# Kernel optimization log

Measured on AMD Instinct MI355X. Metric: run time of the kernel, lower is better.

## Reference

```python
import jax, jax.numpy as jnp
import numpy as np


def _d2(a, b):
    # squared euclidean distances, clamped at 0 (matches _full_cdist before sqrt)
    a2 = jnp.sum(a * a, axis=1)[:, None]
    b2 = jnp.sum(b * b, axis=1)[None, :]
    return jnp.clip(a2 + b2 - 2.0 * (a @ b.T), 0.0, None)


def _node_weights(pts, w1, b1, w2, b2):
    h = jax.nn.relu(pts @ w1 + b1)
    logits = h @ w2 + b2
    w = jax.nn.softplus(logits) + 1e-6
    w = w / jnp.sum(w)
    return w[:, 0]


def setup_inputs() -> dict:
    key = jax.random.key(0)
    ks = jax.random.split(key, 8)
    N, M, D, H, S = 8192, 8192, 2, 32, 3
    return {
        "base_points": jax.random.normal(ks[0], (N, D), jnp.float32),
        "target_points": jax.random.normal(ks[1], (M, D), jnp.float32),
        "log_sigmas": jnp.log(jnp.array([0.05, 0.1, 0.2], jnp.float32)),
        "log_scale": 0.1 * jax.random.normal(ks[2], (D,), jnp.float32),
        "wn_w1": jax.random.normal(ks[3], (D, H), jnp.float32) / np.sqrt(D),
        "wn_b1": jnp.zeros((H,), jnp.float32),
        "wn_w2": jax.random.normal(ks[4], (H, 1), jnp.float32) / np.sqrt(H),
        "wn_b2": jnp.zeros((1,), jnp.float32),
        "g_w1": jax.random.normal(ks[5], (4, H), jnp.float32) / 2.0,
        "g_b1": jnp.zeros((H,), jnp.float32),
        "g_w2": jax.random.normal(ks[6], (H, S), jnp.float32) / np.sqrt(H),
        "g_b2": jnp.zeros((S,), jnp.float32),
        "bias": jnp.zeros((1,), jnp.float32),
    }


def reference(base_points, target_points, log_sigmas, log_scale,
              wn_w1, wn_b1, wn_w2, wn_b2,
              g_w1, g_b1, g_w2, g_b2, bias):
    # learned anisotropic per-axis scale
    scale = jnp.exp(log_scale)
    base = base_points * scale
    target = target_points * scale

    # learned positive, normalized node weights (shared weight_net)
    w_b = _node_weights(base, wn_w1, wn_b1, wn_w2, wn_b2)
    w_t = _node_weights(target, wn_w1, wn_b1, wn_w2, wn_b2)

    # kde_mmd_loss with center=True: subtract weighted mean of each cloud.
    bc = base - jnp.sum(w_b[:, None] * base, axis=0)
    tc = target - jnp.sum(w_t[:, None] * target, axis=0)

    # squared distances computed ONCE, reused across all sigma bands
    d2_aa = _d2(bc, bc)
    d2_bb = _d2(tc, tc)
    d2_ab = _d2(bc, tc)

    sigmas = jnp.exp(log_sigmas)

    def band_loss(sigma):
        inv = 1.0 / (2.0 * sigma * sigma)
        kaa = jnp.exp(-d2_aa * inv)
        kbb = jnp.exp(-d2_bb * inv)
        kab = jnp.exp(-d2_ab * inv)
        # weighted MMD^2: w_a K_aa w_a + w_b K_bb w_b - 2 w_a K_ab w_b
        return (w_b @ (kaa @ w_b) + w_t @ (kbb @ w_t)
                - 2.0 * (w_b @ (kab @ w_t)))

    per_band = jnp.stack([band_loss(sigmas[i]) for i in range(sigmas.shape[0])])

    # gating statistics (torch.tensor([...]) detaches -> stop_gradient)
    dist = jnp.sqrt(_d2(base, target))
    mean_dist = jnp.mean(dist)
    var_dist = jnp.var(dist, ddof=1)  # torch .var() is unbiased
    n_base = base_points.shape[0]
    size_diff = abs(float(n_base - target_points.shape[0])) / (n_base + 1e-6)
    weight_var = jnp.var(w_b, ddof=1) + jnp.var(w_t, ddof=1)
    stats = jax.lax.stop_gradient(
        jnp.stack([mean_dist, var_dist,
                   jnp.asarray(size_diff, base.dtype), weight_var]))

    mix_logits = jax.nn.relu(stats @ g_w1 + g_b1) @ g_w2 + g_b2
    gw = jax.nn.softplus(mix_logits)
    gw = gw / jnp.sum(gw)
    return jnp.sum(gw * per_band) + bias[0]
```

## Files before the change

kernel.cpp:

```cpp
#include <hip/hip_runtime.h>
#include <math.h>

#if __has_builtin(__builtin_amdgcn_exp2f)
#define EXP2F(x) __builtin_amdgcn_exp2f(x)
#else
#define EXP2F(x) exp2f(x)
#endif
#if __has_builtin(__builtin_amdgcn_sqrtf)
#define SQRTF(x) __builtin_amdgcn_sqrtf(x)
#else
#define SQRTF(x) sqrtf(x)
#endif

#define NPTS 8192
#define NJ 512
#define TI 512
#define T16 16
#define NTRI 136
#define NBLK (256 + 2 * NTRI)
#define L2E 1.4426950408889634f

__device__ inline double wred_d(double v) {
#pragma unroll
  for (int o = 32; o > 0; o >>= 1) v += __shfl_down(v, o, 64);
  return v;
}

__device__ inline double bred(double v, double* sm) {
  v = wred_d(v);
  __syncthreads();
  if ((threadIdx.x & 63) == 0) sm[threadIdx.x >> 6] = v;
  __syncthreads();
  return sm[0] + sm[1] + sm[2] + sm[3];
}

__device__ inline void slot_reduce(const double* slot, double* smean) {
  if (threadIdx.x < 64) {
    int l = threadIdx.x;
    const double* sl = slot + l * 4;
#pragma unroll
    for (int c = 0; c < 4; ++c) {
      double v = sl[c];
      double vb = (l < 32) ? v : 0.0;
      double vt = (l < 32) ? 0.0 : v;
      vb = wred_d(vb);
      vt = wred_d(vt);
      if (l == 0) {
        smean[c] = vb;
        smean[4 + c] = vt;
      }
    }
  }
}

__global__ __launch_bounds__(256) void prep_kernel(
    const float* __restrict__ base, const float* __restrict__ target,
    const float* __restrict__ log_sigmas, const float* __restrict__ log_scale,
    const float* __restrict__ w1, const float* __restrict__ b1,
    const float* __restrict__ w2, const float* __restrict__ b2,
    float2* __restrict__ pxy, float* __restrict__ pu,
    double* __restrict__ slot, unsigned* __restrict__ ctr, int n) {
  __shared__ double sm[4];
  int gid = blockIdx.x * 256 + threadIdx.x;
  int isT = gid >= n;
  const float* pts = isT ? target : base;
  int idx = isT ? gid - n : gid;
  float ex = __expf(log_scale[0]);
  float ey = __expf(log_scale[1]);
  float s2 = __expf(log_sigmas[2]);
  float r2 = __fsqrt_rn(L2E / (2.f * s2 * s2));
  float2 p = ((const float2*)pts)[idx];
  float xr = p.x * ex, yr = p.y * ey;
  float logit = b2[0];
#pragma unroll
  for (int k = 0; k < 32; ++k) {
    float h = fmaf(xr, w1[k], fmaf(yr, w1[32 + k], b1[k]));
    h = fmaxf(h, 0.f);
    logit = fmaf(h, w2[k], logit);
  }
  float u = fmaxf(logit, 0.f) + log1pf(__expf(-fabsf(logit))) + 1e-6f;
  float X = xr * r2, Y = yr * r2;
  pxy[gid] = make_float2(X, Y);
  pu[gid] = u;
  double su = bred((double)u, sm);
  double qu = bred((double)u * (double)u, sm);
  double mx = bred((double)u * (double)X, sm);
  double my = bred((double)u * (double)Y, sm);
  if (threadIdx.x == 0) {
    double* s = slot + blockIdx.x * 4;
    s[0] = su;
    s[1] = qu;
    s[2] = mx;
    s[3] = my;
    if (blockIdx.x == 0) *ctr = 0u;
  }
}

template <bool AB, bool FAST>
__device__ inline void tile_loop(const float4* sxy4, const float2* su2,
                                 const float2* sb2, float x0, float y0,
                                 float x1, float y1, float al0, float al1,
                                 float rr0, float rr1, float acc[2][3],
                                 float& sdo, float& sqo) {
  float sd = 0.f, sq = 0.f;
#pragma unroll 2
  for (int jj = 0; jj < NJ / 2; ++jj) {
    float4 xy = sxy4[jj];
    float2 u2 = su2[jj];
    float bj[2];
    if constexpr (AB) {
      float2 b2v = sb2[jj];
      bj[0] = b2v.x;
      bj[1] = b2v.y;
    }
    float xj[2] = {xy.x, xy.z};
    float yj[2] = {xy.y, xy.w};
    float uj[2] = {u2.x, u2.y};
#pragma unroll
    for (int q = 0; q < 2; ++q) {
#pragma unroll
      for (int i = 0; i < 2; ++i) {
        float dx = (i ? x1 : x0) - xj[q];
        float dy = (i ? y1 : y0) - yj[q];
        float s = fmaf(dy, dy, dx * dx);
        float k2 = EXP2F(-s);
        float k0, k1;
        if constexpr (FAST) {
          float t = k2 * k2;
          k1 = t * t;
          float t1 = k1 * k1;
          k0 = t1 * t1;
        } else {
          k1 = EXP2F(-s * rr1);
          k0 = EXP2F(-s * rr0);
        }
        acc[i][0] = fmaf(uj[q], k0, acc[i][0]);
        acc[i][1] = fmaf(uj[q], k1, acc[i][1]);
        acc[i][2] = fmaf(uj[q], k2, acc[i][2]);
        if constexpr (AB) {
          float d2u = fmaxf((s + (i ? al1 : al0)) - bj[q], 0.f);
          sd += SQRTF(d2u);
          sq += d2u;
        }
      }
    }
  }
  sdo = sd;
  sqo = sq;
}

__global__ __launch_bounds__(256) void pair_kernel(
    const float2* __restrict__ pxy, const float* __restrict__ pu,
    const double* __restrict__ slot, double* __restrict__ paa,
    double* __restrict__ pbb, double* __restrict__ pab,
    double* __restrict__ psd, double* __restrict__ psq,
    unsigned* __restrict__ ctr, const float* __restrict__ log_sigmas,
    const float* __restrict__ g_w1, const float* __restrict__ g_b1,
    const float* __restrict__ g_w2, const float* __restrict__ g_b2,
    const float* __restrict__ bias, float* __restrict__ out, int n) {
  __shared__ __align__(16) float2 sxy[NJ];
  __shared__ float su[NJ];
  __shared__ float sb[NJ];
  __shared__ double sm[4];
  __shared__ double smean[8];
  __shared__ int lastf;

  int b = blockIdx.x, m, it, jt, pidx;
  if (b < 256) {
    m = 2;
    pidx = b;
    it = b >> 4;
    jt = b & 15;
  } else {
    int r = b - 256;
    m = (r < NTRI) ? 0 : 1;
    pidx = (m == 0) ? r : r - NTRI;
    int idx = pidx;
    it = 0;
    for (;;) {
      int len = T16 - it;
      if (idx < len) {
        jt = it + idx;
        break;
      }
      idx -= len;
      ++it;
    }
  }
  const float2* pxyI = pxy + ((m == 1) ? n : 0);
  const float* puI = pu + ((m == 1) ? n : 0);
  const float2* pxyJ = pxy + ((m == 0) ? 0 : n);
  const float* puJ = pu + ((m == 0) ? 0 : n);

  int j0 = jt * NJ;
  for (int t = threadIdx.x; t < NJ; t += 256) {
    sxy[t] = pxyJ[j0 + t];
    su[t] = puJ[j0 + t];
  }
  if (m == 2) slot_reduce(slot, smean);
  __syncthreads();

  float cx = 0.f, cy = 0.f;
  if (m == 2) {
    cx = (float)(smean[2] / smean[0] - smean[6] / smean[4]);
    cy = (float)(smean[3] / smean[0] - smean[7] / smean[4]);
    for (int t = threadIdx.x; t < NJ; t += 256) {
      float2 v = sxy[t];
      sb[t] = 2.f * fmaf(cx, v.x, cy * v.y);
    }
    __syncthreads();
  }

  int i0 = it * TI + threadIdx.x;
  float2 P0 = pxyI[i0], P1 = pxyI[i0 + 256];
  float u0 = puI[i0], u1 = puI[i0 + 256];
  float x0 = P0.x - cx, y0 = P0.y - cy;
  float x1 = P1.x - cx, y1 = P1.y - cy;
  float al0 = fmaf(2.f * cx, x0, 2.f * cy * y0) + cx * cx + cy * cy;
  float al1 = fmaf(2.f * cx, x1, 2.f * cy * y1) + cx * cx + cy * cy;

  float s0 = __expf(log_sigmas[0]);
  float s1 = __expf(log_sigmas[1]);
  float s2 = __expf(log_sigmas[2]);
  float rr0 = (s2 * s2) / (s0 * s0);
  float rr1 = (s2 * s2) / (s1 * s1);
  bool fast = (fabsf(rr0 - 16.f) <= 0.016f) && (fabsf(rr1 - 4.f) <= 0.004f);

  float acc[2][3] = {};
  float sd = 0.f, sq = 0.f;
  const float4* sxy4 = reinterpret_cast<const float4*>(sxy);
  const float2* su2 = reinterpret_cast<const float2*>(su);
  const float2* sb2 = reinterpret_cast<const float2*>(sb);
  if (m == 2) {
    if (fast)
      tile_loop<true, true>(sxy4, su2, sb2, x0, y0, x1, y1, al0, al1, rr0, rr1,
                            acc, sd, sq);
    else
      tile_loop<true, false>(sxy4, su2, sb2, x0, y0, x1, y1, al0, al1, rr0,
                             rr1, acc, sd, sq);
  } else {
    if (fast)
      tile_loop<false, true>(sxy4, su2, sb2, x0, y0, x1, y1, al0, al1, rr0,
                             rr1, acc, sd, sq);
    else
      tile_loop<false, false>(sxy4, su2, sb2, x0, y0, x1, y1, al0, al1, rr0,
                              rr1, acc, sd, sq);
  }

  double wgt = (m != 2 && it != jt) ? 2.0 : 1.0;
  double c0 = (double)u0 * (double)acc[0][0] + (double)u1 * (double)acc[1][0];
  double c1 = (double)u0 * (double)acc[0][1] + (double)u1 * (double)acc[1][1];
  double c2 = (double)u0 * (double)acc[0][2] + (double)u1 * (double)acc[1][2];
  double r0 = bred(c0, sm) * wgt;
  double r1 = bred(c1, sm) * wgt;
  double r2d = bred(c2, sm) * wgt;
  double* prow = (m == 0) ? paa : (m == 1) ? pbb : pab;
  int stride = (m == 2) ? 256 : NTRI;
  if (threadIdx.x == 0) {
    prow[0 * stride + pidx] = r0;
    prow[1 * stride + pidx] = r1;
    prow[2 * stride + pidx] = r2d;
  }
  if (m == 2) {
    double rsd = bred((double)sd, sm);
    double rsq = bred((double)sq, sm);
    if (threadIdx.x == 0) {
      psd[pidx] = rsd;
      psq[pidx] = rsq;
    }
  }

  if (threadIdx.x == 0) {
    __threadfence();
    unsigned old = atomicAdd(ctr, 1u);
    lastf = (old == NBLK - 1) ? 1 : 0;
  }
  __syncthreads();
  if (lastf == 0) return;
  __threadfence();

  slot_reduce(slot, smean);
  __syncthreads();
  int t = threadIdx.x;
  double vaa[3], vbb[3], vab[3];
  for (int s = 0; s < 3; ++s) {
    vaa[s] = bred((t < NTRI) ? paa[s * NTRI + t] : 0.0, sm);
    vbb[s] = bred((t < NTRI) ? pbb[s * NTRI + t] : 0.0, sm);
    vab[s] = bred(pab[s * 256 + t], sm);
  }
  double sdt = bred(psd[t], sm);
  double sqt = bred(psq[t], sm);

  if (threadIdx.x == 0) {
    double Sb = smean[0], Qb = smean[1], St = smean[4], Qt = smean[5];
    double pband[3];
    for (int s = 0; s < 3; ++s)
      pband[s] = vaa[s] / (Sb * Sb) + vbb[s] / (St * St) -
                 2.0 * vab[s] / (Sb * St);
    double s2d = (double)s2;
    double r2sq = (double)L2E / (2.0 * s2d * s2d);
    double sd_real = sdt / sqrt(r2sq);
    double sq_real = sqt / r2sq;
    double NN = (double)n;
    double NM = NN * NN;
    double mean_d = sd_real / NM;
    double var_d = (sq_real - sd_real * sd_real / NM) / (NM - 1.0);
    double wv = (Qb / (Sb * Sb) - 1.0 / NN) / (NN - 1.0) +
                (Qt / (St * St) - 1.0 / NN) / (NN - 1.0);
    float st[4] = {(float)mean_d, (float)var_d, 0.f, (float)wv};
    float gl[3] = {g_b2[0], g_b2[1], g_b2[2]};
    for (int k = 0; k < 32; ++k) {
      float h = g_b1[k];
      for (int c = 0; c < 4; ++c) h = fmaf(st[c], g_w1[c * 32 + k], h);
      h = fmaxf(h, 0.f);
      for (int s = 0; s < 3; ++s) gl[s] = fmaf(h, g_w2[k * 3 + s], gl[s]);
    }
    float gw[3];
    float gsum = 0.f;
    for (int s = 0; s < 3; ++s) {
      gw[s] = fmaxf(gl[s], 0.f) + log1pf(__expf(-fabsf(gl[s])));
      gsum += gw[s];
    }
    double r = 0.0;
    for (int s = 0; s < 3; ++s) r += (double)(gw[s] / gsum) * pband[s];
    out[0] = (float)(r + (double)bias[0]);
  }
}

extern "C" void kernel_launch(void* const* d_in, const int* in_sizes, int n_in,
                              void* d_out, int out_size, void* d_ws,
                              size_t ws_size, hipStream_t stream) {
  const float* base = (const float*)d_in[0];
  const float* target = (const float*)d_in[1];
  const float* log_sigmas = (const float*)d_in[2];
  const float* log_scale = (const float*)d_in[3];
  const float* wn_w1 = (const float*)d_in[4];
  const float* wn_b1 = (const float*)d_in[5];
  const float* wn_w2 = (const float*)d_in[6];
  const float* wn_b2 = (const float*)d_in[7];
  const float* g_w1 = (const float*)d_in[8];
  const float* g_b1 = (const float*)d_in[9];
  const float* g_w2 = (const float*)d_in[10];
  const float* g_b2 = (const float*)d_in[11];
  const float* bias = (const float*)d_in[12];
  int n = in_sizes[0] / 2;

  double* dbase = (double*)d_ws;
  double* slot = dbase;
  double* paa = dbase + 256;
  double* pbb = paa + 3 * NTRI;
  double* pab = pbb + 3 * NTRI;
  double* psd = pab + 3 * 256;
  double* psq = psd + 256;
  double* dend = psq + 256;
  float2* pxy = (float2*)dend;
  float* pu = (float*)(pxy + 2 * n);
  unsigned* ctr = (unsigned*)(pu + 2 * n);

  prep_kernel<<<(2 * n) / 256, 256, 0, stream>>>(
      base, target, log_sigmas, log_scale, wn_w1, wn_b1, wn_w2, wn_b2, pxy, pu,
      slot, ctr, n);
  pair_kernel<<<NBLK, 256, 0, stream>>>(pxy, pu, slot, paa, pbb, pab, psd, psq,
                                        ctr, log_sigmas, g_w1, g_b1, g_w2,
                                        g_b2, bias, (float*)d_out, n);
}
```

Measured before the change: 165.9 us.

## Use persistent blocks with atomic job queue and fine-grained 64-column tiles

Replaces the fixed grid of 528 blocks (each handling a 512x512 tile) with 1024 persistent blocks that pull small 512x64 jobs from a global atomic counter. Partial sums are accumulated into a few global doubles with atomicAdd instead of per-block slots reduced by the last block. The aim is better load balance and occupancy across CUs. In exchange it adds per-job synchronisation, reduction and atomic overhead, plus more redundant loading of the i-side points.

```diff
diff --git a/kernel.cpp b/kernel.cpp
--- a/kernel.cpp
+++ b/kernel.cpp
@@ -13,12 +13,16 @@
 #endif
 
 #define NPTS 8192
-#define NJ 512
-#define TI 512
+#define JT 64
+#define ITILE 512
 #define T16 16
 #define NTRI 136
-#define NBLK (256 + 2 * NTRI)
+#define NJOB_AB 2048
+#define NJOB_TRI 1088
+#define NJOBS (NJOB_AB + 2 * NJOB_TRI)
+#define NBLK_PAIR 1024
 #define L2E 1.4426950408889634f
+
 
 __device__ inline double wred_d(double v) {
 #pragma unroll
@@ -59,7 +63,8 @@
     const float* __restrict__ w1, const float* __restrict__ b1,
     const float* __restrict__ w2, const float* __restrict__ b2,
     float2* __restrict__ pxy, float* __restrict__ pu,
-    double* __restrict__ slot, unsigned* __restrict__ ctr, int n) {
+    double* __restrict__ slot, double* __restrict__ acc,
+    unsigned* __restrict__ jctr, unsigned* __restrict__ fctr, int n) {
   __shared__ double sm[4];
   int gid = blockIdx.x * 256 + threadIdx.x;
   int isT = gid >= n;
@@ -92,7 +97,11 @@
     s[1] = qu;
     s[2] = mx;
     s[3] = my;
-    if (blockIdx.x == 0) *ctr = 0u;
+    if (blockIdx.x == 0) {
+      for (int i = 0; i < 11; ++i) acc[i] = 0.0;
+      *jctr = 0u;
+      *fctr = 0u;
+    }
   }
 }
 
@@ -104,7 +113,7 @@
                                  float& sdo, float& sqo) {
   float sd = 0.f, sq = 0.f;
 #pragma unroll 2
-  for (int jj = 0; jj < NJ / 2; ++jj) {
+  for (int jj = 0; jj < JT / 2; ++jj) {
     float4 xy = sxy4[jj];
     float2 u2 = su2[jj];
     float bj[2];
@@ -149,75 +158,28 @@
   sqo = sq;
 }
 
-__global__ __launch_bounds__(256) void pair_kernel(
+__global__ __launch_bounds__(256, 4) void pair_kernel(
     const float2* __restrict__ pxy, const float* __restrict__ pu,
-    const double* __restrict__ slot, double* __restrict__ paa,
-    double* __restrict__ pbb, double* __restrict__ pab,
-    double* __restrict__ psd, double* __restrict__ psq,
-    unsigned* __restrict__ ctr, const float* __restrict__ log_sigmas,
-    const float* __restrict__ g_w1, const float* __restrict__ g_b1,
-    const float* __restrict__ g_w2, const float* __restrict__ g_b2,
-    const float* __restrict__ bias, float* __restrict__ out, int n) {
-  __shared__ __align__(16) float2 sxy[NJ];
-  __shared__ float su[NJ];
-  __shared__ float sb[NJ];
+    const double* __restrict__ slot, double* __restrict__ acc,
+    unsigned* __restrict__ jctr, unsigned* __restrict__ fctr,
+    const float* __restrict__ log_sigmas, const float* __restrict__ g_w1,
+    const float* __restrict__ g_b1, const float* __restrict__ g_w2,
+    const float* __restrict__ g_b2, const float* __restrict__ bias,
+    float* __restrict__ out, int n) {
+  __shared__ __align__(16) float2 sxy[JT];
+  __shared__ __align__(16) float su[JT];
+  __shared__ __align__(16) float sb[JT];
   __shared__ double sm[4];
   __shared__ double smean[8];
+  __shared__ int sjid;
   __shared__ int lastf;
 
-  int b = blockIdx.x, m, it, jt, pidx;
-  if (b < 256) {
-    m = 2;
-    pidx = b;
-    it = b >> 4;
-    jt = b & 15;
-  } else {
-    int r = b - 256;
-    m = (r < NTRI) ? 0 : 1;
-    pidx = (m == 0) ? r : r - NTRI;
-    int idx = pidx;
-    it = 0;
-    for (;;) {
-      int len = T16 - it;
-      if (idx < len) {
-        jt = it + idx;
-        break;
-      }
-      idx -= len;
-      ++it;
-    }
-  }
-  const float2* pxyI = pxy + ((m == 1) ? n : 0);
-  const float* puI = pu + ((m == 1) ? n : 0);
-  const float2* pxyJ = pxy + ((m == 0) ? 0 : n);
-  const float* puJ = pu + ((m == 0) ? 0 : n);
-
-  int j0 = jt * NJ;
-  for (int t = threadIdx.x; t < NJ; t += 256) {
-    sxy[t] = pxyJ[j0 + t];
-    su[t] = puJ[j0 + t];
-  }
-  if (m == 2) slot_reduce(slot, smean);
+  slot_reduce(slot, smean);
   __syncthreads();
-
-  float cx = 0.f, cy = 0.f;
-  if (m == 2) {
-    cx = (float)(smean[2] / smean[0] - smean[6] / smean[4]);
-    cy = (float)(smean[3] / smean[0] - smean[7] / smean[4]);
-    for (int t = threadIdx.x; t < NJ; t += 256) {
-      float2 v = sxy[t];
-      sb[t] = 2.f * fmaf(cx, v.x, cy * v.y);
-    }
-    __syncthreads();
-  }
-
-  int i0 = it * TI + threadIdx.x;
-  float2 P0 = pxyI[i0], P1 = pxyI[i0 + 256];
-  float u0 = puI[i0], u1 = puI[i0 + 256];
-  float x0 = P0.x - cx, y0 = P0.y - cy;
-  float x1 = P1.x - cx, y1 = P1.y - cy;
-  float al0 = fmaf(2.f * cx, x0, 2.f * cy * y0) + cx * cx + cy * cy;
-  float al1 = fmaf(2.f * cx, x1, 2.f * cy * y1) + cx * cx + cy * cy;
+  float cx = (float)(smean[2] / smean[0] - smean[6] / smean[4]);
+  float cy = (float)(smean[3] / smean[0] - smean[7] / smean[4]);
+  float cx2 = 2.f * cx, cy2 = 2.f * cy;
+  float cc = cx * cx + cy * cy;
 
   float s0 = __expf(log_sigmas[0]);
   float s1 = __expf(log_sigmas[1]);
@@ -226,81 +188,122 @@
   float rr1 = (s2 * s2) / (s1 * s1);
   bool fast = (fabsf(rr0 - 16.f) <= 0.016f) && (fabsf(rr1 - 4.f) <= 0.004f);
 
-  float acc[2][3] = {};
-  float sd = 0.f, sq = 0.f;
-  const float4* sxy4 = reinterpret_cast<const float4*>(sxy);
-  const float2* su2 = reinterpret_cast<const float2*>(su);
-  const float2* sb2 = reinterpret_cast<const float2*>(sb);
-  if (m == 2) {
-    if (fast)
-      tile_loop<true, true>(sxy4, su2, sb2, x0, y0, x1, y1, al0, al1, rr0, rr1,
-                            acc, sd, sq);
-    else
-      tile_loop<true, false>(sxy4, su2, sb2, x0, y0, x1, y1, al0, al1, rr0,
-                             rr1, acc, sd, sq);
-  } else {
-    if (fast)
-      tile_loop<false, true>(sxy4, su2, sb2, x0, y0, x1, y1, al0, al1, rr0,
-                             rr1, acc, sd, sq);
-    else
-      tile_loop<false, false>(sxy4, su2, sb2, x0, y0, x1, y1, al0, al1, rr0,
-                              rr1, acc, sd, sq);
-  }
-
-  double wgt = (m != 2 && it != jt) ? 2.0 : 1.0;
-  double c0 = (double)u0 * (double)acc[0][0] + (double)u1 * (double)acc[1][0];
-  double c1 = (double)u0 * (double)acc[0][1] + (double)u1 * (double)acc[1][1];
-  double c2 = (double)u0 * (double)acc[0][2] + (double)u1 * (double)acc[1][2];
-  double r0 = bred(c0, sm) * wgt;
-  double r1 = bred(c1, sm) * wgt;
-  double r2d = bred(c2, sm) * wgt;
-  double* prow = (m == 0) ? paa : (m == 1) ? pbb : pab;
-  int stride = (m == 2) ? 256 : NTRI;
-  if (threadIdx.x == 0) {
-    prow[0 * stride + pidx] = r0;
-    prow[1 * stride + pidx] = r1;
-    prow[2 * stride + pidx] = r2d;
-  }
-  if (m == 2) {
-    double rsd = bred((double)sd, sm);
-    double rsq = bred((double)sq, sm);
+  for (;;) {
+    __syncthreads();
+    if (threadIdx.x == 0) sjid = (int)atomicAdd(jctr, 1u);
+    __syncthreads();
+    int job = sjid;
+    if (job >= NJOBS) break;
+
+    int m, it, jt = 0, j0;
+    if (job < NJOB_AB) {
+      m = 2;
+      it = job >> 7;
+      j0 = (job & 127) * JT;
+    } else {
+      int r = job - NJOB_AB;
+      m = (r < NJOB_TRI) ? 0 : 1;
+      if (m == 1) r -= NJOB_TRI;
+      int tri = r >> 3;
+      int q = r & 7;
+      int idx = tri, len = T16;
+      it = 0;
+      while (idx >= len) {
+        idx -= len;
+        --len;
+        ++it;
+      }
+      jt = it + idx;
+      j0 = jt * ITILE + q * JT;
+    }
+    const float2* pxyI = pxy + ((m == 1) ? n : 0);
+    const float* puI = pu + ((m == 1) ? n : 0);
+    const float2* pxyJ = pxy + ((m == 0) ? 0 : n);
+    const float* puJ = pu + ((m == 0) ? 0 : n);
+
+    if (threadIdx.x < JT) {
+      float2 v = pxyJ[j0 + threadIdx.x];
+      sxy[threadIdx.x] = v;
+      su[threadIdx.x] = puJ[j0 + threadIdx.x];
+      if (m == 2) sb[threadIdx.x] = fmaf(cx2, v.x, cy2 * v.y);
+    }
+    __syncthreads();
+
+    int i0 = it * ITILE + threadIdx.x;
+    float2 P0 = pxyI[i0], P1 = pxyI[i0 + 256];
+    float u0 = puI[i0], u1 = puI[i0 + 256];
+    float x0 = P0.x, y0 = P0.y, x1 = P1.x, y1 = P1.y;
+    float al0 = 0.f, al1 = 0.f;
+    if (m == 2) {
+      x0 -= cx; y0 -= cy; x1 -= cx; y1 -= cy;
+      al0 = fmaf(cx2, x0, cy2 * y0) + cc;
+      al1 = fmaf(cx2, x1, cy2 * y1) + cc;
+    }
+
+    float accf[2][3] = {};
+    float sd = 0.f, sq = 0.f;
+    const float4* sxy4 = reinterpret_cast<const float4*>(sxy);
+    const float2* su2 = reinterpret_cast<const float2*>(su);
+    const float2* sb2 = reinterpret_cast<const float2*>(sb);
+    if (m == 2) {
+      if (fast)
+        tile_loop<true, true>(sxy4, su2, sb2, x0, y0, x1, y1, al0, al1, rr0,
+                              rr1, accf, sd, sq);
+      else
+        tile_loop<true, false>(sxy4, su2, sb2, x0, y0, x1, y1, al0, al1, rr0,
+                               rr1, accf, sd, sq);
+    } else {
+      if (fast)
+        tile_loop<false, true>(sxy4, su2, sb2, x0, y0, x1, y1, al0, al1, rr0,
+                               rr1, accf, sd, sq);
+      else
+        tile_loop<false, false>(sxy4, su2, sb2, x0, y0, x1, y1, al0, al1, rr0,
+                                rr1, accf, sd, sq);
+    }
+
+    double wgt = (m != 2 && jt != it) ? 2.0 : 1.0;
+    double c0 = (double)u0 * accf[0][0] + (double)u1 * accf[1][0];
+    double c1 = (double)u0 * accf[0][1] + (double)u1 * accf[1][1];
+    double c2 = (double)u0 * accf[0][2] + (double)u1 * accf[1][2];
+    double r0 = bred(c0, sm) * wgt;
+    double r1 = bred(c1, sm) * wgt;
+    double r2d = bred(c2, sm) * wgt;
     if (threadIdx.x == 0) {
-      psd[pidx] = rsd;
-      psq[pidx] = rsq;
+      atomicAdd(&acc[3 * m + 0], r0);
+      atomicAdd(&acc[3 * m + 1], r1);
+      atomicAdd(&acc[3 * m + 2], r2d);
+    }
+    if (m == 2) {
+      double rsd = bred((double)sd, sm);
+      double rsq = bred((double)sq, sm);
+      if (threadIdx.x == 0) {
+        atomicAdd(&acc[9], rsd);
+        atomicAdd(&acc[10], rsq);
+      }
     }
   }
 
   if (threadIdx.x == 0) {
     __threadfence();
-    unsigned old = atomicAdd(ctr, 1u);
-    lastf = (old == NBLK - 1) ? 1 : 0;
+    unsigned old = atomicAdd(fctr, 1u);
+    lastf = (old == NBLK_PAIR - 1) ? 1 : 0;
   }
   __syncthreads();
-  if (lastf == 0) return;
+  if (!lastf) return;
   __threadfence();
 
-  slot_reduce(slot, smean);
-  __syncthreads();
-  int t = threadIdx.x;
-  double vaa[3], vbb[3], vab[3];
-  for (int s = 0; s < 3; ++s) {
-    vaa[s] = bred((t < NTRI) ? paa[s * NTRI + t] : 0.0, sm);
-    vbb[s] = bred((t < NTRI) ? pbb[s * NTRI + t] : 0.0, sm);
-    vab[s] = bred(pab[s * 256 + t], sm);
-  }
-  double sdt = bred(psd[t], sm);
-  double sqt = bred(psq[t], sm);
-
   if (threadIdx.x == 0) {
+    double v[11];
+    for (int i = 0; i < 11; ++i) v[i] = atomicAdd(&acc[i], 0.0);
     double Sb = smean[0], Qb = smean[1], St = smean[4], Qt = smean[5];
     double pband[3];
     for (int s = 0; s < 3; ++s)
-      pband[s] = vaa[s] / (Sb * Sb) + vbb[s] / (St * St) -
-                 2.0 * vab[s] / (Sb * St);
+      pband[s] = v[s] / (Sb * Sb) + v[3 + s] / (St * St) -
+                 2.0 * v[6 + s] / (Sb * St);
     double s2d = (double)s2;
     double r2sq = (double)L2E / (2.0 * s2d * s2d);
-    double sd_real = sdt / sqrt(r2sq);
-    double sq_real = sqt / r2sq;
+    double sd_real = v[9] / sqrt(r2sq);
+    double sq_real = v[10] / r2sq;
     double NN = (double)n;
     double NM = NN * NN;
     double mean_d = sd_real / NM;
@@ -347,20 +350,17 @@
 
   double* dbase = (double*)d_ws;
   double* slot = dbase;
-  double* paa = dbase + 256;
-  double* pbb = paa + 3 * NTRI;
-  double* pab = pbb + 3 * NTRI;
-  double* psd = pab + 3 * 256;
-  double* psq = psd + 256;
-  double* dend = psq + 256;
+  double* acc = dbase + 256;
+  double* dend = acc + 12;
   float2* pxy = (float2*)dend;
   float* pu = (float*)(pxy + 2 * n);
-  unsigned* ctr = (unsigned*)(pu + 2 * n);
+  unsigned* jctr = (unsigned*)(pu + 2 * n);
+  unsigned* fctr = jctr + 1;
 
   prep_kernel<<<(2 * n) / 256, 256, 0, stream>>>(
       base, target, log_sigmas, log_scale, wn_w1, wn_b1, wn_w2, wn_b2, pxy, pu,
-      slot, ctr, n);
-  pair_kernel<<<NBLK, 256, 0, stream>>>(pxy, pu, slot, paa, pbb, pab, psd, psq,
-                                        ctr, log_sigmas, g_w1, g_b1, g_w2,
-                                        g_b2, bias, (float*)d_out, n);
-}
+      slot, acc, jctr, fctr, n);
+  pair_kernel<<<NBLK_PAIR, 256, 0, stream>>>(pxy, pu, slot, acc, jctr, fctr,
+                                             log_sigmas, g_w1, g_b1, g_w2,
+                                             g_b2, bias, (float*)d_out, n);
+}
```

Result: slower. 264.0 us (+59.1%).

## Retile pair kernel into many small J-chunk jobs with four rows per thread

Applied to the files above, without the earlier changes.

Replaces the 512x512 tile blocks (528 blocks) with 1024-row I tiles split into 64-wide J chunks, giving 2176 blocks, and has each thread handle four I points instead of two. The goal is better load balance and occupancy across the GPU's compute units, and more register reuse of each J point loaded from shared memory. In exchange, each block recomputes its setup, loads its I points and runs a full set of block reductions and an atomic over only 64 J columns. The final reduction is widened to cover the larger partial arrays.

```diff
diff --git a/kernel.cpp b/kernel.cpp
--- a/kernel.cpp
+++ b/kernel.cpp
@@ -13,11 +13,14 @@
 #endif
 
 #define NPTS 8192
-#define NJ 512
-#define TI 512
-#define T16 16
-#define NTRI 136
-#define NBLK (256 + 2 * NTRI)
+#define JT 64
+#define ITILE 1024
+#define T8 8
+#define NTRI8 36
+#define JCH 16
+#define NJOB_AB 1024
+#define NJOB_TRI 576
+#define NBLK (NJOB_AB + 2 * NJOB_TRI)
 #define L2E 1.4426950408889634f
 
 __device__ inline double wred_d(double v) {
@@ -59,7 +62,7 @@
     const float* __restrict__ w1, const float* __restrict__ b1,
     const float* __restrict__ w2, const float* __restrict__ b2,
     float2* __restrict__ pxy, float* __restrict__ pu,
-    double* __restrict__ slot, unsigned* __restrict__ ctr, int n) {
+    double* __restrict__ slot, unsigned* __restrict__ fctr, int n) {
   __shared__ double sm[4];
   int gid = blockIdx.x * 256 + threadIdx.x;
   int isT = gid >= n;
@@ -92,19 +95,19 @@
     s[1] = qu;
     s[2] = mx;
     s[3] = my;
-    if (blockIdx.x == 0) *ctr = 0u;
+    if (blockIdx.x == 0) *fctr = 0u;
   }
 }
 
 template <bool AB, bool FAST>
 __device__ inline void tile_loop(const float4* sxy4, const float2* su2,
-                                 const float2* sb2, float x0, float y0,
-                                 float x1, float y1, float al0, float al1,
-                                 float rr0, float rr1, float acc[2][3],
+                                 const float2* sb2, const float x[4],
+                                 const float y[4], const float al[4],
+                                 float rr0, float rr1, float acc[4][3],
                                  float& sdo, float& sqo) {
   float sd = 0.f, sq = 0.f;
 #pragma unroll 2
-  for (int jj = 0; jj < NJ / 2; ++jj) {
+  for (int jj = 0; jj < JT / 2; ++jj) {
     float4 xy = sxy4[jj];
     float2 u2 = su2[jj];
     float bj[2];
@@ -119,9 +122,9 @@
 #pragma unroll
     for (int q = 0; q < 2; ++q) {
 #pragma unroll
-      for (int i = 0; i < 2; ++i) {
-        float dx = (i ? x1 : x0) - xj[q];
-        float dy = (i ? y1 : y0) - yj[q];
+      for (int i = 0; i < 4; ++i) {
+        float dx = x[i] - xj[q];
+        float dy = y[i] - yj[q];
         float s = fmaf(dy, dy, dx * dx);
         float k2 = EXP2F(-s);
         float k0, k1;
@@ -138,7 +141,7 @@
         acc[i][1] = fmaf(uj[q], k1, acc[i][1]);
         acc[i][2] = fmaf(uj[q], k2, acc[i][2]);
         if constexpr (AB) {
-          float d2u = fmaxf((s + (i ? al1 : al0)) - bj[q], 0.f);
+          float d2u = fmaxf((s + al[i]) - bj[q], 0.f);
           sd += SQRTF(d2u);
           sq += d2u;
         }
@@ -154,70 +157,50 @@
     const double* __restrict__ slot, double* __restrict__ paa,
     double* __restrict__ pbb, double* __restrict__ pab,
     double* __restrict__ psd, double* __restrict__ psq,
-    unsigned* __restrict__ ctr, const float* __restrict__ log_sigmas,
+    unsigned* __restrict__ fctr, const float* __restrict__ log_sigmas,
     const float* __restrict__ g_w1, const float* __restrict__ g_b1,
     const float* __restrict__ g_w2, const float* __restrict__ g_b2,
     const float* __restrict__ bias, float* __restrict__ out, int n) {
-  __shared__ __align__(16) float2 sxy[NJ];
-  __shared__ float su[NJ];
-  __shared__ float sb[NJ];
+  __shared__ __align__(16) float2 sxy[JT];
+  __shared__ __align__(16) float su[JT];
+  __shared__ __align__(16) float sb[JT];
   __shared__ double sm[4];
   __shared__ double smean[8];
   __shared__ int lastf;
 
-  int b = blockIdx.x, m, it, jt, pidx;
-  if (b < 256) {
+  int b = blockIdx.x;
+  int m, it, jt = 0, j0, pidx;
+  if (b < NJOB_AB) {
     m = 2;
     pidx = b;
-    it = b >> 4;
-    jt = b & 15;
+    it = b >> 7;
+    j0 = (b & 127) * JT;
   } else {
-    int r = b - 256;
-    m = (r < NTRI) ? 0 : 1;
-    pidx = (m == 0) ? r : r - NTRI;
-    int idx = pidx;
+    int r = b - NJOB_AB;
+    m = (r < NJOB_TRI) ? 0 : 1;
+    if (m == 1) r -= NJOB_TRI;
+    pidx = r;
+    int tile = r >> 4;
+    int q = r & 15;
+    int idx = tile, len = T8;
     it = 0;
-    for (;;) {
-      int len = T16 - it;
-      if (idx < len) {
-        jt = it + idx;
-        break;
-      }
+    while (idx >= len) {
       idx -= len;
+      --len;
       ++it;
     }
+    jt = it + idx;
+    j0 = jt * ITILE + q * JT;
   }
   const float2* pxyI = pxy + ((m == 1) ? n : 0);
   const float* puI = pu + ((m == 1) ? n : 0);
   const float2* pxyJ = pxy + ((m == 0) ? 0 : n);
   const float* puJ = pu + ((m == 0) ? 0 : n);
 
-  int j0 = jt * NJ;
-  for (int t = threadIdx.x; t < NJ; t += 256) {
-    sxy[t] = pxyJ[j0 + t];
-    su[t] = puJ[j0 + t];
-  }
-  if (m == 2) slot_reduce(slot, smean);
-  __syncthreads();
-
-  float cx = 0.f, cy = 0.f;
+  float cx = 0.f, cy = 0.f, cx2 = 0.f, cy2 = 0.f, cc = 0.f;
   if (m == 2) {
-    cx = (float)(smean[2] / smean[0] - smean[6] / smean[4]);
-    cy = (float)(smean[3] / smean[0] - smean[7] / smean[4]);
-    for (int t = threadIdx.x; t < NJ; t += 256) {
-      float2 v = sxy[t];
-      sb[t] = 2.f * fmaf(cx, v.x, cy * v.y);
-    }
-    __syncthreads();
-  }
-
-  int i0 = it * TI + threadIdx.x;
-  float2 P0 = pxyI[i0], P1 = pxyI[i0 + 256];
-  float u0 = puI[i0], u1 = puI[i0 + 256];
-  float x0 = P0.x - cx, y0 = P0.y - cy;
-  float x1 = P1.x - cx, y1 = P1.y - cy;
-  float al0 = fmaf(2.f * cx, x0, 2.f * cy * y0) + cx * cx + cy * cy;
-  float al1 = fmaf(2.f * cx, x1, 2.f * cy * y1) + cx * cx + cy * cy;
+    slot_reduce(slot, smean);
+  }
 
   float s0 = __expf(log_sigmas[0]);
   float s1 = __expf(log_sigmas[1]);
@@ -226,36 +209,70 @@
   float rr1 = (s2 * s2) / (s1 * s1);
   bool fast = (fabsf(rr0 - 16.f) <= 0.016f) && (fabsf(rr1 - 4.f) <= 0.004f);
 
-  float acc[2][3] = {};
+  if (m == 2) {
+    __syncthreads();
+    cx = (float)(smean[2] / smean[0] - smean[6] / smean[4]);
+    cy = (float)(smean[3] / smean[0] - smean[7] / smean[4]);
+    cx2 = 2.f * cx;
+    cy2 = 2.f * cy;
+    cc = cx * cx + cy * cy;
+  }
+
+  if (threadIdx.x < JT) {
+    float2 v = pxyJ[j0 + threadIdx.x];
+    sxy[threadIdx.x] = v;
+    su[threadIdx.x] = puJ[j0 + threadIdx.x];
+    if (m == 2) sb[threadIdx.x] = fmaf(cx2, v.x, cy2 * v.y);
+  }
+  __syncthreads();
+
+  int i0 = it * ITILE + threadIdx.x;
+  float x[4], y[4], u[4], al[4];
+#pragma unroll
+  for (int i = 0; i < 4; ++i) {
+    float2 P = pxyI[i0 + i * 256];
+    u[i] = puI[i0 + i * 256];
+    x[i] = P.x;
+    y[i] = P.y;
+    al[i] = 0.f;
+    if (m == 2) {
+      x[i] -= cx;
+      y[i] -= cy;
+      al[i] = fmaf(cx2, x[i], cy2 * y[i]) + cc;
+    }
+  }
+
+  float accf[4][3] = {};
   float sd = 0.f, sq = 0.f;
   const float4* sxy4 = reinterpret_cast<const float4*>(sxy);
   const float2* su2 = reinterpret_cast<const float2*>(su);
   const float2* sb2 = reinterpret_cast<const float2*>(sb);
   if (m == 2) {
     if (fast)
-      tile_loop<true, true>(sxy4, su2, sb2, x0, y0, x1, y1, al0, al1, rr0, rr1,
-                            acc, sd, sq);
+      tile_loop<true, true>(sxy4, su2, sb2, x, y, al, rr0, rr1, accf, sd, sq);
     else
-      tile_loop<true, false>(sxy4, su2, sb2, x0, y0, x1, y1, al0, al1, rr0,
-                             rr1, acc, sd, sq);
+      tile_loop<true, false>(sxy4, su2, sb2, x, y, al, rr0, rr1, accf, sd, sq);
   } else {
     if (fast)
-      tile_loop<false, true>(sxy4, su2, sb2, x0, y0, x1, y1, al0, al1, rr0,
-                             rr1, acc, sd, sq);
+      tile_loop<false, true>(sxy4, su2, sb2, x, y, al, rr0, rr1, accf, sd, sq);
     else
-      tile_loop<false, false>(sxy4, su2, sb2, x0, y0, x1, y1, al0, al1, rr0,
-                              rr1, acc, sd, sq);
-  }
-
-  double wgt = (m != 2 && it != jt) ? 2.0 : 1.0;
-  double c0 = (double)u0 * (double)acc[0][0] + (double)u1 * (double)acc[1][0];
-  double c1 = (double)u0 * (double)acc[0][1] + (double)u1 * (double)acc[1][1];
-  double c2 = (double)u0 * (double)acc[0][2] + (double)u1 * (double)acc[1][2];
+      tile_loop<false, false>(sxy4, su2, sb2, x, y, al, rr0, rr1, accf, sd,
+                              sq);
+  }
+
+  double wgt = (m != 2 && jt != it) ? 2.0 : 1.0;
+  double c0 = 0.0, c1 = 0.0, c2 = 0.0;
+#pragma unroll
+  for (int i = 0; i < 4; ++i) {
+    c0 += (double)u[i] * accf[i][0];
+    c1 += (double)u[i] * accf[i][1];
+    c2 += (double)u[i] * accf[i][2];
+  }
   double r0 = bred(c0, sm) * wgt;
   double r1 = bred(c1, sm) * wgt;
   double r2d = bred(c2, sm) * wgt;
   double* prow = (m == 0) ? paa : (m == 1) ? pbb : pab;
-  int stride = (m == 2) ? 256 : NTRI;
+  int stride = (m == 2) ? NJOB_AB : NJOB_TRI;
   if (threadIdx.x == 0) {
     prow[0 * stride + pidx] = r0;
     prow[1 * stride + pidx] = r1;
@@ -272,11 +289,11 @@
 
   if (threadIdx.x == 0) {
     __threadfence();
-    unsigned old = atomicAdd(ctr, 1u);
+    unsigned old = atomicAdd(fctr, 1u);
     lastf = (old == NBLK - 1) ? 1 : 0;
   }
   __syncthreads();
-  if (lastf == 0) return;
+  if (!lastf) return;
   __threadfence();
 
   slot_reduce(slot, smean);
@@ -284,12 +301,18 @@
   int t = threadIdx.x;
   double vaa[3], vbb[3], vab[3];
   for (int s = 0; s < 3; ++s) {
-    vaa[s] = bred((t < NTRI) ? paa[s * NTRI + t] : 0.0, sm);
-    vbb[s] = bred((t < NTRI) ? pbb[s * NTRI + t] : 0.0, sm);
-    vab[s] = bred(pab[s * 256 + t], sm);
-  }
-  double sdt = bred(psd[t], sm);
-  double sqt = bred(psq[t], sm);
+    const double* pa = paa + s * NJOB_TRI;
+    const double* pb = pbb + s * NJOB_TRI;
+    const double* pc = pab + s * NJOB_AB;
+    double va = pa[t] + pa[t + 256] + ((t < 64) ? pa[t + 512] : 0.0);
+    double vb = pb[t] + pb[t + 256] + ((t < 64) ? pb[t + 512] : 0.0);
+    double vc = pc[t] + pc[t + 256] + pc[t + 512] + pc[t + 768];
+    vaa[s] = bred(va, sm);
+    vbb[s] = bred(vb, sm);
+    vab[s] = bred(vc, sm);
+  }
+  double sdt = bred(psd[t] + psd[t + 256] + psd[t + 512] + psd[t + 768], sm);
+  double sqt = bred(psq[t] + psq[t + 256] + psq[t + 512] + psq[t + 768], sm);
 
   if (threadIdx.x == 0) {
     double Sb = smean[0], Qb = smean[1], St = smean[4], Qt = smean[5];
@@ -348,19 +371,19 @@
   double* dbase = (double*)d_ws;
   double* slot = dbase;
   double* paa = dbase + 256;
-  double* pbb = paa + 3 * NTRI;
-  double* pab = pbb + 3 * NTRI;
-  double* psd = pab + 3 * 256;
-  double* psq = psd + 256;
-  double* dend = psq + 256;
+  double* pbb = paa + 3 * NJOB_TRI;
+  double* pab = pbb + 3 * NJOB_TRI;
+  double* psd = pab + 3 * NJOB_AB;
+  double* psq = psd + NJOB_AB;
+  double* dend = psq + NJOB_AB;
   float2* pxy = (float2*)dend;
   float* pu = (float*)(pxy + 2 * n);
-  unsigned* ctr = (unsigned*)(pu + 2 * n);
+  unsigned* fctr = (unsigned*)(pu + 2 * n);
 
   prep_kernel<<<(2 * n) / 256, 256, 0, stream>>>(
       base, target, log_sigmas, log_scale, wn_w1, wn_b1, wn_w2, wn_b2, pxy, pu,
-      slot, ctr, n);
+      slot, fctr, n);
   pair_kernel<<<NBLK, 256, 0, stream>>>(pxy, pu, slot, paa, pbb, pab, psd, psq,
-                                        ctr, log_sigmas, g_w1, g_b1, g_w2,
+                                        fctr, log_sigmas, g_w1, g_b1, g_w2,
                                         g_b2, bias, (float*)d_out, n);
 }
```

After: 158.6 us. 1.05x faster.
